# Kernel optimization log

Measured on AMD Instinct MI355X. Metric: run time of the kernel, lower is better.

The kernel has to match this reference:

```python
import jax, jax.numpy as jnp
import numpy as np

D_MODEL = 1024
N_HEADS = 2
D_FF = 4096
SEQ = 4096
HEAD_DIM = D_MODEL // N_HEADS
SCALE = HEAD_DIM ** 0.5
LN_EPS = 1e-5


def _layer_norm(x, g, b):
    mu = jnp.mean(x, axis=-1, keepdims=True)
    var = jnp.mean(jnp.square(x - mu), axis=-1, keepdims=True)
    return (x - mu) * jax.lax.rsqrt(var + LN_EPS) * g + b


def _gelu_tanh(x):
    # torch nn.GELU(approximate='tanh')
    c = np.sqrt(2.0 / np.pi).astype(np.float32)
    return 0.5 * x * (1.0 + jnp.tanh(c * (x + 0.044715 * x * x * x)))


def setup_inputs() -> dict:
    key = jax.random.key(0)
    ks = jax.random.split(key, 12)
    s = 1.0 / np.sqrt(D_MODEL)
    sf = 1.0 / np.sqrt(D_FF)
    inp = {
        "x": jax.random.normal(ks[0], (SEQ, D_MODEL), jnp.float32),
        "ln1_g": jnp.ones((D_MODEL,), jnp.float32),
        "ln1_b": jnp.zeros((D_MODEL,), jnp.float32),
        "wq": jax.random.normal(ks[1], (D_MODEL, D_MODEL), jnp.float32) * s,
        "bq": jnp.zeros((D_MODEL,), jnp.float32),
        "wk": jax.random.normal(ks[2], (D_MODEL, D_MODEL), jnp.float32) * s,
        "bk": jnp.zeros((D_MODEL,), jnp.float32),
        "wv": jax.random.normal(ks[3], (D_MODEL, D_MODEL), jnp.float32) * s,
        "bv": jnp.zeros((D_MODEL,), jnp.float32),
        "wo": jax.random.normal(ks[4], (D_MODEL, D_MODEL), jnp.float32) * s,
        "bo": jnp.zeros((D_MODEL,), jnp.float32),
        "ln2_g": jnp.ones((D_MODEL,), jnp.float32),
        "ln2_b": jnp.zeros((D_MODEL,), jnp.float32),
        "w1": jax.random.normal(ks[5], (D_FF, D_MODEL), jnp.float32) * s,
        "b1": jnp.zeros((D_FF,), jnp.float32),
        "w2": jax.random.normal(ks[6], (D_MODEL, D_FF), jnp.float32) * sf,
        "b2": jnp.zeros((D_MODEL,), jnp.float32),
    }
    return inp


def reference(x, ln1_g, ln1_b, wq, bq, wk, bk, wv, bv, wo, bo,
              ln2_g, ln2_b, w1, b1, w2, b2):
    S = x.shape[0]
    h = _layer_norm(x, ln1_g, ln1_b)
    # torch Linear: y = h @ W.T + b
    q = h @ wq.T + bq
    k = h @ wk.T + bk
    v = h @ wv.T + bv
    # chunk(2, dim=-1) == reshape last dim to (heads, head_dim)
    qh = q.reshape(S, N_HEADS, HEAD_DIM)
    kh = k.reshape(S, N_HEADS, HEAD_DIM)
    vh = v.reshape(S, N_HEADS, HEAD_DIM)
    scores = jnp.einsum('shd,thd->hst', qh, kh) / SCALE  # [H,S,S]
    attn = jax.nn.softmax(scores, axis=-1)
    o = jnp.einsum('hst,thd->shd', attn, vh).reshape(S, D_MODEL)
    x = x + (o @ wo.T + bo)
    h2 = _layer_norm(x, ln2_g, ln2_b)
    ff = _gelu_tanh(h2 @ w1.T + b1) @ w2.T + b2
    return x + ff
```

## Files before the change

### kernel.cpp

```cpp
#include <hip/hip_runtime.h>
#include <math.h>

#define SEQ 4096
#define DM  1024
#define DFF 4096
#define NH  2
#define HD  512

typedef unsigned short ushort_t;
typedef short  s16x8 __attribute__((ext_vector_type(8)));
typedef float  f32x4 __attribute__((ext_vector_type(4)));

__device__ __forceinline__ float bf2f(unsigned short u) {
    return __uint_as_float(((unsigned)u) << 16);
}
__device__ __forceinline__ unsigned short f2bf(float f) {
    unsigned u = __float_as_uint(f);
    unsigned r = (u + 0x7fffu + ((u >> 16) & 1u)) >> 16;
    return (unsigned short)r;
}

__device__ __forceinline__ void async_load16(void* lds, const void* g) {
    __builtin_amdgcn_global_load_lds(
        (const __attribute__((address_space(1))) void*)g,
        (__attribute__((address_space(3))) void*)lds, 16, 0, 0);
}

template<bool HAS_BIAS, bool DO_GELU, bool HAS_RES, bool OUT_BF16, int SPLITS,
         int MODE, int BM, bool TRV>
__global__ __launch_bounds__(BM == 256 ? 512 : 256)
void gemm_nt(const ushort_t* __restrict__ A, int lda,
             const ushort_t* __restrict__ B, int ldb,
             void* __restrict__ Cv, int ldc,
             const float* __restrict__ bias,
             const float* __restrict__ res, int ldres,
             int K, float alpha,
             size_t strA, size_t strB, size_t strC, size_t strBias,
             float* __restrict__ rowsum, ushort_t* __restrict__ vt)
{
    __shared__ alignas(16) ushort_t sA[BM * 64];
    __shared__ alignas(16) ushort_t sB[128 * 64];

    const int z  = blockIdx.z;
    const int zb = z / SPLITS;
    const int ks = (z % SPLITS) * K;
    A += (size_t)zb * strA;
    B += (size_t)zb * strB;
    if (HAS_BIAS) bias += (size_t)zb * strBias;

    const int tid   = threadIdx.x;
    const int lane  = tid & 63;
    const int wave  = tid >> 6;
    const int waveM = wave >> 1, waveN = wave & 1;
    const int m0 = blockIdx.y * BM, n0 = blockIdx.x * 128;
    const int lr = lane & 15, quad = lane >> 4;

    f32x4 acc[4][4] = {};

    const ushort_t* Ag = A + (size_t)m0 * lda + ks;
    const ushort_t* Bg = B + (size_t)n0 * ldb + ks;

    const int ldRow = (lane >> 3);
    const int ldCol = (((lane & 7) ^ (lane >> 3)) * 8);
    const int NB = (BM == 256) ? 2 : 4;
    const int BW = (BM == 256) ? 16 : 32;

    for (int k0 = 0; k0 < K; k0 += 64) {
#pragma unroll
        for (int i = 0; i < 4; ++i) {
            async_load16(&sA[(wave * 32 + i * 8) * 64],
                         Ag + (size_t)(wave * 32 + i * 8 + ldRow) * lda + k0 + ldCol);
        }
#pragma unroll
        for (int i = 0; i < NB; ++i) {
            async_load16(&sB[(wave * BW + i * 8) * 64],
                         Bg + (size_t)(wave * BW + i * 8 + ldRow) * ldb + k0 + ldCol);
        }
        __syncthreads();

#pragma unroll
        for (int kk = 0; kk < 64; kk += 32) {
            const int pg = ((((kk >> 3) + quad) ^ (lr & 7)) << 3);
            s16x8 af[4], bfr[4];
#pragma unroll
            for (int mi = 0; mi < 4; ++mi)
                af[mi] = *(const s16x8*)&sA[(waveM * 64 + mi * 16 + lr) * 64 + pg];
#pragma unroll
            for (int ni = 0; ni < 4; ++ni)
                bfr[ni] = *(const s16x8*)&sB[(waveN * 64 + ni * 16 + lr) * 64 + pg];
#pragma unroll
            for (int mi = 0; mi < 4; ++mi)
#pragma unroll
                for (int ni = 0; ni < 4; ++ni)
                    acc[mi][ni] = __builtin_amdgcn_mfma_f32_16x16x32_bf16(
                        af[mi], bfr[ni], acc[mi][ni], 0, 0, 0);
        }
        __syncthreads();
    }

    if (TRV && zb == 2) {
#pragma unroll
        for (int mi = 0; mi < 4; ++mi) {
#pragma unroll
            for (int ni = 0; ni < 4; ++ni) {
                int t0 = m0 + waveM * 64 + mi * 16 + quad * 4;
                int col = n0 + waveN * 64 + ni * 16 + lr;
                unsigned b[4];
#pragma unroll
                for (int r = 0; r < 4; ++r) {
                    float v = acc[mi][ni][r] * alpha;
                    if (HAS_BIAS) v += bias[col];
                    b[r] = f2bf(v);
                }
                uint2 pk;
                pk.x = b[0] | (b[1] << 16);
                pk.y = b[2] | (b[3] << 16);
                int h = col >> 9, d = col & (HD - 1);
                *(uint2*)(vt + (size_t)h * HD * SEQ + (size_t)d * SEQ + t0) = pk;
            }
        }
        return;
    }

    float rs_part[4][4];
    if (MODE == 1) {
#pragma unroll
        for (int mi = 0; mi < 4; ++mi)
#pragma unroll
            for (int r = 0; r < 4; ++r) rs_part[mi][r] = 0.0f;
    }

#pragma unroll
    for (int mi = 0; mi < 4; ++mi) {
#pragma unroll
        for (int r = 0; r < 4; ++r) {
            int row = m0 + waveM * 64 + mi * 16 + quad * 4 + r;
#pragma unroll
            for (int ni = 0; ni < 4; ++ni) {
                int col = n0 + waveN * 64 + ni * 16 + lr;
                float v = acc[mi][ni][r] * alpha;
                if (HAS_BIAS) v += bias[col];
                if (DO_GELU) {
                    float xx = v;
                    float y2 = 1.5957691216057308f * (xx + 0.044715f * xx * xx * xx);
                    float t = __expf(y2);
                    v = xx * t / (t + 1.0f);
                }
                if (HAS_RES) v += res[(size_t)row * ldres + col];
                if (OUT_BF16) {
                    ushort_t bs = f2bf(MODE == 1 ? __expf(v) : v);
                    if (MODE == 1) rs_part[mi][r] += bf2f(bs);
                    ((ushort_t*)Cv)[(size_t)z * strC + (size_t)row * ldc + col] = bs;
                } else {
                    ((float*)Cv)[(size_t)z * strC + (size_t)row * ldc + col] = v;
                }
            }
        }
    }

    if (MODE == 1) {
#pragma unroll
        for (int mi = 0; mi < 4; ++mi) {
#pragma unroll
            for (int r = 0; r < 4; ++r) {
                float s = rs_part[mi][r];
                s += __shfl_xor(s, 1);
                s += __shfl_xor(s, 2);
                s += __shfl_xor(s, 4);
                s += __shfl_xor(s, 8);
                if (lr == 0) {
                    int row = m0 + waveM * 64 + mi * 16 + quad * 4 + r;
                    atomicAdd(&rowsum[(size_t)zb * SEQ + row], s);
                }
            }
        }
    }
}

template<int S, bool HAS_BIAS, bool HAS_RES, bool OUT_BF16, bool DIV_RS>
__global__ __launch_bounds__(256)
void reduce_splitk(const float* __restrict__ P, size_t slab,
                   void* __restrict__ outv, int N, int ldout, int colStride,
                   const float* __restrict__ bias,
                   const float* __restrict__ res, int ldres,
                   const float* __restrict__ rowsum)
{
    const int z = blockIdx.z;
    const float* Pz = P + (size_t)z * S * slab;
    size_t i = ((size_t)blockIdx.x * 256 + threadIdx.x) * 4;
    if (i >= slab) return;
    int row = (int)(i / (size_t)N);
    int col = (int)(i - (size_t)row * N);
    float4 a = *(const float4*)(Pz + i);
#pragma unroll
    for (int s = 1; s < S; ++s) {
        float4 b = *(const float4*)(Pz + (size_t)s * slab + i);
        a.x += b.x; a.y += b.y; a.z += b.z; a.w += b.w;
    }
    if (DIV_RS) {
        float inv = 1.0f / rowsum[(size_t)z * SEQ + row];
        a.x *= inv; a.y *= inv; a.z *= inv; a.w *= inv;
    }
    int oc = z * colStride + col;
    if (HAS_BIAS) {
        a.x += bias[oc]; a.y += bias[oc + 1]; a.z += bias[oc + 2]; a.w += bias[oc + 3];
    }
    if (HAS_RES) {
        float4 r4 = *(const float4*)(res + (size_t)row * ldres + oc);
        a.x += r4.x; a.y += r4.y; a.z += r4.z; a.w += r4.w;
    }
    if (OUT_BF16) {
        ushort_t* o = (ushort_t*)outv + (size_t)row * ldout + oc;
        o[0] = f2bf(a.x); o[1] = f2bf(a.y); o[2] = f2bf(a.z); o[3] = f2bf(a.w);
    } else {
        *(float4*)((float*)outv + (size_t)row * ldout + oc) = a;
    }
}

__global__ __launch_bounds__(256)
void reduce_oproj_ln(const float* __restrict__ P,
                     const float* __restrict__ bo, const float* __restrict__ x,
                     float* __restrict__ X1,
                     const float* __restrict__ g, const float* __restrict__ b,
                     ushort_t* __restrict__ H)
{
    int row = blockIdx.x;
    int tid = threadIdx.x;
    size_t off = (size_t)row * DM + tid * 4;
    float4 p0 = *(const float4*)(P + off);
    float4 p1 = *(const float4*)(P + (size_t)SEQ * DM + off);
    float4 bb = ((const float4*)bo)[tid];
    float4 xr = *(const float4*)(x + off);
    float4 v;
    v.x = p0.x + p1.x + bb.x + xr.x;
    v.y = p0.y + p1.y + bb.y + xr.y;
    v.z = p0.z + p1.z + bb.z + xr.z;
    v.w = p0.w + p1.w + bb.w + xr.w;
    *(float4*)(X1 + off) = v;

    float s1 = v.x + v.y + v.z + v.w;
    float s2 = v.x * v.x + v.y * v.y + v.z * v.z + v.w * v.w;
#pragma unroll
    for (int o = 32; o > 0; o >>= 1) {
        s1 += __shfl_down(s1, o);
        s2 += __shfl_down(s2, o);
    }
    __shared__ float r1[4], r2[4];
    if ((tid & 63) == 0) { r1[tid >> 6] = s1; r2[tid >> 6] = s2; }
    __syncthreads();
    s1 = r1[0] + r1[1] + r1[2] + r1[3];
    s2 = r2[0] + r2[1] + r2[2] + r2[3];
    float mu  = s1 * (1.0f / DM);
    float var = s2 * (1.0f / DM) - mu * mu;
    float rs  = rsqrtf(var + 1e-5f);
    float4 gg = ((const float4*)g)[tid];
    float4 be = ((const float4*)b)[tid];
    ushort_t* o = H + off;
    o[0] = f2bf((v.x - mu) * rs * gg.x + be.x);
    o[1] = f2bf((v.y - mu) * rs * gg.y + be.y);
    o[2] = f2bf((v.z - mu) * rs * gg.z + be.z);
    o[3] = f2bf((v.w - mu) * rs * gg.w + be.w);
}

__global__ __launch_bounds__(256)
void prep_ln(const float* __restrict__ wq, const float* __restrict__ wk,
             const float* __restrict__ wv, const float* __restrict__ wo,
             const float* __restrict__ w1, const float* __restrict__ w2,
             ushort_t* __restrict__ WQ, ushort_t* __restrict__ WK,
             ushort_t* __restrict__ WV, ushort_t* __restrict__ WO,
             ushort_t* __restrict__ W1d, ushort_t* __restrict__ W2d,
             const float* __restrict__ bq, const float* __restrict__ bk,
             const float* __restrict__ bv, float* __restrict__ BQKV,
             float* __restrict__ RSUM,
             const float* __restrict__ x, const float* __restrict__ g1,
             const float* __restrict__ be1, ushort_t* __restrict__ H)
{
    int tid = threadIdx.x;
    if (blockIdx.x < SEQ) {
        int row = blockIdx.x;
        float4 v = ((const float4*)(x + (size_t)row * DM))[tid];
        float s1 = v.x + v.y + v.z + v.w;
        float s2 = v.x * v.x + v.y * v.y + v.z * v.z + v.w * v.w;
#pragma unroll
        for (int o = 32; o > 0; o >>= 1) {
            s1 += __shfl_down(s1, o);
            s2 += __shfl_down(s2, o);
        }
        __shared__ float r1[4], r2[4];
        if ((tid & 63) == 0) { r1[tid >> 6] = s1; r2[tid >> 6] = s2; }
        __syncthreads();
        s1 = r1[0] + r1[1] + r1[2] + r1[3];
        s2 = r2[0] + r2[1] + r2[2] + r2[3];
        float mu  = s1 * (1.0f / DM);
        float var = s2 * (1.0f / DM) - mu * mu;
        float rs  = rsqrtf(var + 1e-5f);
        float4 gg = ((const float4*)g1)[tid];
        float4 bb = ((const float4*)be1)[tid];
        ushort_t* o = H + (size_t)row * DM + tid * 4;
        o[0] = f2bf((v.x - mu) * rs * gg.x + bb.x);
        o[1] = f2bf((v.y - mu) * rs * gg.y + bb.y);
        o[2] = f2bf((v.z - mu) * rs * gg.z + bb.z);
        o[3] = f2bf((v.w - mu) * rs * gg.w + bb.w);
        return;
    }

    const long S1   = (long)DM * DM / 4;
    const long SW   = 4 * S1;
    const long SBIG = (long)DFF * DM / 4;
    long i = (long)(blockIdx.x - SEQ) * 256 + tid;

    const float* src; ushort_t* dst; long off;
    if (i < SW) {
        long seg = i / S1; off = i - seg * S1;
        src = seg == 0 ? wq : seg == 1 ? wk : seg == 2 ? wv : wo;
        dst = seg == 0 ? WQ : seg == 1 ? WK : seg == 2 ? WV : WO;
    } else if (i < SW + SBIG) {
        off = i - SW; src = w1; dst = W1d;
    } else if (i < SW + 2 * SBIG) {
        off = i - SW - SBIG; src = w2; dst = W2d;
    } else {
        long j = i - (SW + 2 * SBIG);
        if (j < 3 * DM / 4) {
            long e = j * 4;
#pragma unroll
            for (int t = 0; t < 4; ++t) {
                long k = e + t;
                float v = k < DM ? bq[k] : k < 2 * DM ? bk[k - DM] : bv[k - 2 * DM];
                BQKV[k] = v;
            }
        } else if (j < 3 * DM / 4 + NH * SEQ / 4) {
            long k = (j - 3 * DM / 4) * 4;
            *(float4*)&RSUM[k] = make_float4(0.f, 0.f, 0.f, 0.f);
        }
        return;
    }
    float4 f = *(const float4*)(src + off * 4);
    ushort_t* d = dst + off * 4;
    d[0] = f2bf(f.x); d[1] = f2bf(f.y); d[2] = f2bf(f.z); d[3] = f2bf(f.w);
}

extern "C" void kernel_launch(void* const* d_in, const int* in_sizes, int n_in,
                              void* d_out, int out_size, void* d_ws, size_t ws_size,
                              hipStream_t stream)
{
    const float* x   = (const float*)d_in[0];
    const float* g1  = (const float*)d_in[1];
    const float* be1 = (const float*)d_in[2];
    const float* wq  = (const float*)d_in[3];
    const float* bq  = (const float*)d_in[4];
    const float* wk  = (const float*)d_in[5];
    const float* bk  = (const float*)d_in[6];
    const float* wv  = (const float*)d_in[7];
    const float* bv  = (const float*)d_in[8];
    const float* wo  = (const float*)d_in[9];
    const float* bo  = (const float*)d_in[10];
    const float* g2  = (const float*)d_in[11];
    const float* be2 = (const float*)d_in[12];
    const float* w1  = (const float*)d_in[13];
    const float* b1  = (const float*)d_in[14];
    const float* w2  = (const float*)d_in[15];
    const float* b2  = (const float*)d_in[16];
    float* out = (float*)d_out;

    char* ws = (char*)d_ws;
    const size_t MB = 1ull << 20;
    ushort_t* WQ   = (ushort_t*)(ws + 0 * MB);
    ushort_t* WK   = (ushort_t*)(ws + 2 * MB);
    ushort_t* WV   = (ushort_t*)(ws + 4 * MB);
    ushort_t* WO   = (ushort_t*)(ws + 6 * MB);
    ushort_t* W1   = (ushort_t*)(ws + 8 * MB);
    ushort_t* W2   = (ushort_t*)(ws + 16 * MB);
    ushort_t* H    = (ushort_t*)(ws + 24 * MB);
    ushort_t* Q    = (ushort_t*)(ws + 32 * MB);
    ushort_t* Kb   = (ushort_t*)(ws + 40 * MB);
    ushort_t* Vt   = (ushort_t*)(ws + 56 * MB);
    ushort_t* SC   = (ushort_t*)(ws + 64 * MB);
    ushort_t* O    = (ushort_t*)(ws + 128 * MB);
    float*    X1   = (float*)(ws + 136 * MB);
    float*    P    = (float*)(ws + 152 * MB);
    float*    BQKV = (float*)(ws + 216 * MB);
    float*    RSUM = (float*)(ws + 216 * MB + 16 * 1024);

    dim3 blk(256), blk2(512);

    {
        long total = 4L * DM * DM + 2L * DFF * DM;
        long n4 = total / 4 + 3 * DM / 4 + NH * SEQ / 4;
        unsigned prepBlocks = (unsigned)((n4 + 255) / 256);
        prep_ln<<<dim3(SEQ + prepBlocks), blk, 0, stream>>>(
            wq, wk, wv, wo, w1, w2, WQ, WK, WV, WO, W1, W2,
            bq, bk, bv, BQKV, RSUM, x, g1, be1, H);
    }

    gemm_nt<true, false, false, true, 1, 0, 256, true>
        <<<dim3(DM / 128, SEQ / 256, 3), blk2, 0, stream>>>(
        H, DM, WQ, DM, Q, DM, BQKV, nullptr, 0, DM, 1.0f,
        0, (size_t)DM * DM, (size_t)SEQ * DM, (size_t)DM, nullptr, Vt);

    const float scale = 0.044194173824159216f;
    gemm_nt<false, false, false, true, 1, 1, 256, false>
        <<<dim3(SEQ / 128, SEQ / 256, NH), blk2, 0, stream>>>(
        Q, DM, Kb, DM, SC, SEQ, nullptr, nullptr, 0, HD, scale,
        (size_t)HD, (size_t)HD, (size_t)SEQ * SEQ, 0, RSUM, nullptr);

    gemm_nt<false, false, false, false, 2, 0, 128, false>
        <<<dim3(HD / 128, SEQ / 128, NH * 2), blk, 0, stream>>>(
        SC, SEQ, Vt, SEQ, P, HD, nullptr, nullptr, 0, SEQ / 2, 1.0f,
        (size_t)SEQ * SEQ, (size_t)HD * SEQ, (size_t)SEQ * HD, 0, nullptr, nullptr);
    reduce_splitk<2, false, false, true, true>
        <<<dim3((SEQ * HD / 4) / 256, 1, NH), blk, 0, stream>>>(
        P, (size_t)SEQ * HD, O, HD, DM, HD, nullptr, nullptr, 0, RSUM);

    gemm_nt<false, false, false, false, 2, 0, 128, false>
        <<<dim3(DM / 128, SEQ / 128, 2), blk, 0, stream>>>(
        O, DM, WO, DM, P, DM, nullptr, nullptr, 0, DM / 2, 1.0f,
        0, 0, (size_t)SEQ * DM, 0, nullptr, nullptr);
    reduce_oproj_ln<<<SEQ, 256, 0, stream>>>(P, bo, x, X1, g2, be2, H);

    ushort_t* F1 = SC;
    gemm_nt<true, true, false, true, 1, 0, 256, false>
        <<<dim3(DFF / 128, SEQ / 256, 1), blk2, 0, stream>>>(
        H, DM, W1, DM, F1, DFF, b1, nullptr, 0, DM, 1.0f, 0, 0, 0, 0,
        nullptr, nullptr);

    gemm_nt<false, false, false, false, 2, 0, 128, false>
        <<<dim3(DM / 128, SEQ / 128, 2), blk, 0, stream>>>(
        F1, DFF, W2, DFF, P, DM, nullptr, nullptr, 0, DFF / 2, 1.0f,
        0, 0, (size_t)SEQ * DM, 0, nullptr, nullptr);
    reduce_splitk<2, true, true, false, false>
        <<<dim3((SEQ * DM / 4) / 256, 1, 1), blk, 0, stream>>>(
        P, (size_t)SEQ * DM, out, DM, DM, 0, b2, X1, DM, nullptr);
}
```

Measured before the change: 399.4 us.

## Add 4-wave fat-tile GEMM kernel for QKV, scores and FFN1

Introduces gemm_fat, which computes a 256x128 tile with 4 waves instead of 8. Each wave owns a 64x128 sub-tile with 4x8 MFMA accumulators, so every LDS-loaded B fragment is reused across more MFMAs and fewer waves contend for LDS bandwidth. The QKV projection, the score/exp GEMM and the FFN1 GELU GEMM now use it, and the transposed-V and rowsum epilogues move out of gemm_nt into the new kernel. The cost is much higher register pressure (128 accumulator floats per lane) under launch_bounds(256,2), which risks spills or lower occupancy, and fewer waves are left to hide latency.

After: 398.2 us. About the same (-0.3%).

```diff
diff --git a/kernel.cpp b/kernel.cpp
--- a/kernel.cpp
+++ b/kernel.cpp
@@ -24,6 +24,143 @@
     __builtin_amdgcn_global_load_lds(
         (const __attribute__((address_space(1))) void*)g,
         (__attribute__((address_space(3))) void*)lds, 16, 0, 0);
+}
+
+template<bool HAS_BIAS, bool DO_GELU, bool OUT_BF16, int MODE, bool TRV>
+__global__ __launch_bounds__(256, 2)
+void gemm_fat(const ushort_t* __restrict__ A, int lda,
+              const ushort_t* __restrict__ B, int ldb,
+              void* __restrict__ Cv, int ldc,
+              const float* __restrict__ bias,
+              int K, float alpha,
+              size_t strA, size_t strB, size_t strC, size_t strBias,
+              float* __restrict__ rowsum, ushort_t* __restrict__ vt)
+{
+    __shared__ alignas(16) ushort_t sA[256 * 64];
+    __shared__ alignas(16) ushort_t sB[128 * 64];
+
+    const int z = blockIdx.z;
+    A += (size_t)z * strA;
+    B += (size_t)z * strB;
+    if (HAS_BIAS) bias += (size_t)z * strBias;
+
+    const int tid  = threadIdx.x;
+    const int lane = tid & 63;
+    const int wave = tid >> 6;
+    const int m0 = blockIdx.y * 256, n0 = blockIdx.x * 128;
+    const int lr = lane & 15, quad = lane >> 4;
+
+    f32x4 acc[4][8] = {};
+
+    const ushort_t* Ag = A + (size_t)m0 * lda;
+    const ushort_t* Bg = B + (size_t)n0 * ldb;
+
+    const int ldRow = (lane >> 3);
+    const int ldCol = (((lane & 7) ^ (lane >> 3)) * 8);
+
+    for (int k0 = 0; k0 < K; k0 += 64) {
+#pragma unroll
+        for (int i = 0; i < 8; ++i)
+            async_load16(&sA[(wave * 64 + i * 8) * 64],
+                         Ag + (size_t)(wave * 64 + i * 8 + ldRow) * lda + k0 + ldCol);
+#pragma unroll
+        for (int i = 0; i < 4; ++i)
+            async_load16(&sB[(wave * 32 + i * 8) * 64],
+                         Bg + (size_t)(wave * 32 + i * 8 + ldRow) * ldb + k0 + ldCol);
+        __syncthreads();
+
+#pragma unroll
+        for (int kk = 0; kk < 64; kk += 32) {
+            const int pg = ((((kk >> 3) + quad) ^ (lr & 7)) << 3);
+            s16x8 af[4], bfr[8];
+#pragma unroll
+            for (int mi = 0; mi < 4; ++mi)
+                af[mi] = *(const s16x8*)&sA[(wave * 64 + mi * 16 + lr) * 64 + pg];
+#pragma unroll
+            for (int ni = 0; ni < 8; ++ni)
+                bfr[ni] = *(const s16x8*)&sB[(ni * 16 + lr) * 64 + pg];
+#pragma unroll
+            for (int mi = 0; mi < 4; ++mi)
+#pragma unroll
+                for (int ni = 0; ni < 8; ++ni)
+                    acc[mi][ni] = __builtin_amdgcn_mfma_f32_16x16x32_bf16(
+                        af[mi], bfr[ni], acc[mi][ni], 0, 0, 0);
+        }
+        __syncthreads();
+    }
+
+    if (TRV && z == 2) {
+#pragma unroll
+        for (int mi = 0; mi < 4; ++mi) {
+#pragma unroll
+            for (int ni = 0; ni < 8; ++ni) {
+                int t0 = m0 + wave * 64 + mi * 16 + quad * 4;
+                int col = n0 + ni * 16 + lr;
+                unsigned b[4];
+#pragma unroll
+                for (int r = 0; r < 4; ++r) {
+                    float v = acc[mi][ni][r] * alpha;
+                    if (HAS_BIAS) v += bias[col];
+                    b[r] = f2bf(v);
+                }
+                uint2 pk;
+                pk.x = b[0] | (b[1] << 16);
+                pk.y = b[2] | (b[3] << 16);
+                int h = col >> 9, d = col & (HD - 1);
+                *(uint2*)(vt + (size_t)h * HD * SEQ + (size_t)d * SEQ + t0) = pk;
+            }
+        }
+        return;
+    }
+
+    if (MODE == 1) {
+#pragma unroll
+        for (int mi = 0; mi < 4; ++mi) {
+#pragma unroll
+            for (int r = 0; r < 4; ++r) {
+                int row = m0 + wave * 64 + mi * 16 + quad * 4 + r;
+                float s = 0.0f;
+#pragma unroll
+                for (int ni = 0; ni < 8; ++ni) {
+                    int col = n0 + ni * 16 + lr;
+                    ushort_t bs = f2bf(__expf(acc[mi][ni][r] * alpha));
+                    s += bf2f(bs);
+                    ((ushort_t*)Cv)[(size_t)z * strC + (size_t)row * ldc + col] = bs;
+                }
+                s += __shfl_xor(s, 1);
+                s += __shfl_xor(s, 2);
+                s += __shfl_xor(s, 4);
+                s += __shfl_xor(s, 8);
+                if (lr == 0)
+                    atomicAdd(&rowsum[(size_t)z * SEQ + row], s);
+            }
+        }
+        return;
+    }
+
+#pragma unroll
+    for (int mi = 0; mi < 4; ++mi) {
+#pragma unroll
+        for (int r = 0; r < 4; ++r) {
+            int row = m0 + wave * 64 + mi * 16 + quad * 4 + r;
+#pragma unroll
+            for (int ni = 0; ni < 8; ++ni) {
+                int col = n0 + ni * 16 + lr;
+                float v = acc[mi][ni][r] * alpha;
+                if (HAS_BIAS) v += bias[col];
+                if (DO_GELU) {
+                    float xx = v;
+                    float y2 = 1.5957691216057308f * (xx + 0.044715f * xx * xx * xx);
+                    float t = __expf(y2);
+                    v = xx * t / (t + 1.0f);
+                }
+                if (OUT_BF16)
+                    ((ushort_t*)Cv)[(size_t)z * strC + (size_t)row * ldc + col] = f2bf(v);
+                else
+                    ((float*)Cv)[(size_t)z * strC + (size_t)row * ldc + col] = v;
+            }
+        }
+    }
 }
 
 template<bool HAS_BIAS, bool DO_GELU, bool HAS_RES, bool OUT_BF16, int SPLITS,
@@ -98,38 +235,6 @@
         __syncthreads();
     }
 
-    if (TRV && zb == 2) {
-#pragma unroll
-        for (int mi = 0; mi < 4; ++mi) {
-#pragma unroll
-            for (int ni = 0; ni < 4; ++ni) {
-                int t0 = m0 + waveM * 64 + mi * 16 + quad * 4;
-                int col = n0 + waveN * 64 + ni * 16 + lr;
-                unsigned b[4];
-#pragma unroll
-                for (int r = 0; r < 4; ++r) {
-                    float v = acc[mi][ni][r] * alpha;
-                    if (HAS_BIAS) v += bias[col];
-                    b[r] = f2bf(v);
-                }
-                uint2 pk;
-                pk.x = b[0] | (b[1] << 16);
-                pk.y = b[2] | (b[3] << 16);
-                int h = col >> 9, d = col & (HD - 1);
-                *(uint2*)(vt + (size_t)h * HD * SEQ + (size_t)d * SEQ + t0) = pk;
-            }
-        }
-        return;
-    }
-
-    float rs_part[4][4];
-    if (MODE == 1) {
-#pragma unroll
-        for (int mi = 0; mi < 4; ++mi)
-#pragma unroll
-            for (int r = 0; r < 4; ++r) rs_part[mi][r] = 0.0f;
-    }
-
 #pragma unroll
     for (int mi = 0; mi < 4; ++mi) {
 #pragma unroll
@@ -147,31 +252,10 @@
                     v = xx * t / (t + 1.0f);
                 }
                 if (HAS_RES) v += res[(size_t)row * ldres + col];
-                if (OUT_BF16) {
-                    ushort_t bs = f2bf(MODE == 1 ? __expf(v) : v);
-                    if (MODE == 1) rs_part[mi][r] += bf2f(bs);
-                    ((ushort_t*)Cv)[(size_t)z * strC + (size_t)row * ldc + col] = bs;
-                } else {
+                if (OUT_BF16)
+                    ((ushort_t*)Cv)[(size_t)z * strC + (size_t)row * ldc + col] = f2bf(v);
+                else
                     ((float*)Cv)[(size_t)z * strC + (size_t)row * ldc + col] = v;
-                }
-            }
-        }
-    }
-
-    if (MODE == 1) {
-#pragma unroll
-        for (int mi = 0; mi < 4; ++mi) {
-#pragma unroll
-            for (int r = 0; r < 4; ++r) {
-                float s = rs_part[mi][r];
-                s += __shfl_xor(s, 1);
-                s += __shfl_xor(s, 2);
-                s += __shfl_xor(s, 4);
-                s += __shfl_xor(s, 8);
-                if (lr == 0) {
-                    int row = m0 + waveM * 64 + mi * 16 + quad * 4 + r;
-                    atomicAdd(&rowsum[(size_t)zb * SEQ + row], s);
-                }
             }
         }
     }
@@ -381,7 +465,7 @@
     float*    BQKV = (float*)(ws + 216 * MB);
     float*    RSUM = (float*)(ws + 216 * MB + 16 * 1024);
 
-    dim3 blk(256), blk2(512);
+    dim3 blk(256);
 
     {
         long total = 4L * DM * DM + 2L * DFF * DM;
@@ -392,15 +476,15 @@
             bq, bk, bv, BQKV, RSUM, x, g1, be1, H);
     }
 
-    gemm_nt<true, false, false, true, 1, 0, 256, true>
-        <<<dim3(DM / 128, SEQ / 256, 3), blk2, 0, stream>>>(
-        H, DM, WQ, DM, Q, DM, BQKV, nullptr, 0, DM, 1.0f,
+    gemm_fat<true, false, true, 0, true>
+        <<<dim3(DM / 128, SEQ / 256, 3), blk, 0, stream>>>(
+        H, DM, WQ, DM, Q, DM, BQKV, DM, 1.0f,
         0, (size_t)DM * DM, (size_t)SEQ * DM, (size_t)DM, nullptr, Vt);
 
     const float scale = 0.044194173824159216f;
-    gemm_nt<false, false, false, true, 1, 1, 256, false>
-        <<<dim3(SEQ / 128, SEQ / 256, NH), blk2, 0, stream>>>(
-        Q, DM, Kb, DM, SC, SEQ, nullptr, nullptr, 0, HD, scale,
+    gemm_fat<false, false, true, 1, false>
+        <<<dim3(SEQ / 128, SEQ / 256, NH), blk, 0, stream>>>(
+        Q, DM, Kb, DM, SC, SEQ, nullptr, HD, scale,
         (size_t)HD, (size_t)HD, (size_t)SEQ * SEQ, 0, RSUM, nullptr);
 
     gemm_nt<false, false, false, false, 2, 0, 128, false>
@@ -418,10 +502,9 @@
     reduce_oproj_ln<<<SEQ, 256, 0, stream>>>(P, bo, x, X1, g2, be2, H);
 
     ushort_t* F1 = SC;
-    gemm_nt<true, true, false, true, 1, 0, 256, false>
-        <<<dim3(DFF / 128, SEQ / 256, 1), blk2, 0, stream>>>(
-        H, DM, W1, DM, F1, DFF, b1, nullptr, 0, DM, 1.0f, 0, 0, 0, 0,
-        nullptr, nullptr);
+    gemm_fat<true, true, true, 0, false>
+        <<<dim3(DFF / 128, SEQ / 256, 1), blk, 0, stream>>>(
+        H, DM, W1, DM, F1, DFF, b1, DM, 1.0f, 0, 0, 0, 0, nullptr, nullptr);
 
     gemm_nt<false, false, false, false, 2, 0, 128, false>
         <<<dim3(DM / 128, SEQ / 128, 2), blk, 0, stream>>>(
```
